# Performance work log

Measured on AMD Instinct MI355X. Metric: run time of the kernel, lower is better.

## Reference

```python
import jax, jax.numpy as jnp
import numpy as np

B, D_IN, T = 16, 512, 4096
D_CB, K = 8, 1024
COMMITMENT = 1.0


def _weight_norm(v, g):
    # torch weight_norm with dim=0: w[o] = g[o] * v[o] / ||v[o]||
    return g[:, None] * v / jnp.sqrt(jnp.sum(v * v, axis=1, keepdims=True))


def setup_inputs() -> dict:
    key = jax.random.key(0)
    ks = jax.random.split(key, 8)
    return {
        "z": jax.random.normal(ks[0], (B, D_IN, T), dtype=jnp.float32),
        "in_v": jax.random.normal(ks[1], (D_CB, D_IN), dtype=jnp.float32) * 0.05,
        "in_g": jax.random.uniform(ks[2], (D_CB,), dtype=jnp.float32, minval=0.5, maxval=1.5),
        "in_b": jax.random.normal(ks[3], (D_CB,), dtype=jnp.float32) * 0.01,
        "out_v": jax.random.normal(ks[4], (D_IN, D_CB), dtype=jnp.float32) * 0.05,
        "out_g": jax.random.uniform(ks[5], (D_IN,), dtype=jnp.float32, minval=0.5, maxval=1.5),
        "out_b": jax.random.normal(ks[6], (D_IN,), dtype=jnp.float32) * 0.01,
        "codebook": jax.random.normal(ks[7], (K, D_CB), dtype=jnp.float32),
    }


def reference(z, in_v, in_g, in_b, out_v, out_g, out_b, codebook):
    z = z.astype(jnp.float32)
    # in_project: weight-normed 1x1 conv == per-timestep linear [D_IN -> D_CB]
    w_in = _weight_norm(in_v, in_g)                       # [D_CB, D_IN]
    z_e = jnp.einsum('cd,bdt->bct', w_in, z) + in_b[None, :, None]  # [B, D_CB, T]

    enc = jnp.transpose(z_e, (0, 2, 1))                   # [B, T, D_CB]
    cb = codebook.astype(jnp.float32)                     # [K, D_CB]
    # squared euclidean distance via expansion
    d = (jnp.sum(enc * enc, axis=-1, keepdims=True)
         - 2.0 * jnp.einsum('btd,kd->btk', enc, cb)
         + jnp.sum(cb * cb, axis=-1)[None, None, :])      # [B, T, K]
    indices = jnp.argmin(d, axis=-1)                      # [B, T] int

    z_q = jnp.transpose(cb[indices], (0, 2, 1))           # [B, D_CB, T]
    commit_loss = jnp.mean((z_e - jax.lax.stop_gradient(z_q)) ** 2, axis=(1, 2)) * COMMITMENT  # [B]

    # straight-through estimator
    z_q_st = z_e + jax.lax.stop_gradient(z_q - z_e)

    w_out = _weight_norm(out_v, out_g)                    # [D_IN, D_CB]
    out = jnp.einsum('cd,bdt->bct', w_out, z_q_st) + out_b[None, :, None]  # [B, D_IN, T]
    return out, commit_loss, indices
```

## Files before the change

kernel.cpp:

```cpp
#include <hip/hip_runtime.h>
#include <math.h>

#define NB 16
#define DIN 512
#define TT 4096
#define DCB 8
#define KC 1024
#define NW 8
#define TC 128


__global__ __launch_bounds__(512) void vq_setup(
    const float* __restrict__ in_v, const float* __restrict__ in_g,
    const float* __restrict__ out_v, const float* __restrict__ out_g,
    const float* __restrict__ cb, float* __restrict__ ws)
{
    int tid = threadIdx.x;
    float* w_inT = ws;
    float* w_out = ws + 4096;
    float* cb2   = ws + 8192;

    {
        int c    = tid >> 6;
        int lane = tid & 63;
        const float* v = in_v + c * DIN;
        float s = 0.f;
        #pragma unroll
        for (int i = 0; i < DIN; i += 64) {
            float x = v[i + lane];
            s += x * x;
        }
        #pragma unroll
        for (int off = 32; off > 0; off >>= 1) s += __shfl_xor(s, off, 64);
        float sq = sqrtf(s);
        float g  = in_g[c];
        #pragma unroll
        for (int i = 0; i < DIN; i += 64) {
            int d = i + lane;
            w_inT[d * DCB + c] = (g * v[d]) / sq;
        }
    }
    {
        int o = tid;
        const float* v = out_v + o * DCB;
        float s = 0.f;
        #pragma unroll
        for (int c = 0; c < DCB; ++c) s += v[c] * v[c];
        float sq = sqrtf(s);
        float g  = out_g[o];
        #pragma unroll
        for (int c = 0; c < DCB; ++c) w_out[o * DCB + c] = (g * v[c]) / sq;
    }
    for (int k = tid; k < KC; k += 512) {
        const float* r = cb + k * DCB;
        float s = 0.f;
        #pragma unroll
        for (int c = 0; c < DCB; ++c) s += r[c] * r[c];
        cb2[k] = s;
    }
}

__global__ __launch_bounds__(512, 4) void vq_main(
    const float* __restrict__ z, const float* __restrict__ in_b,
    const float* __restrict__ out_b, const float* __restrict__ cb,
    const float* __restrict__ ws, float* __restrict__ ws_commit,
    float* __restrict__ out)
{
    __shared__ float s_cb[KC * DCB];
    __shared__ float s_cb2[KC];
    __shared__ float s_red[NW * DCB * TC];
    __shared__ float s_sd[NW][TC];
    __shared__ int   s_si[NW][TC];

    const float* w_inT = ws;
    const float* w_out = ws + 4096;

    int tid  = threadIdx.x;
    int w    = tid >> 6;
    int wu   = __builtin_amdgcn_readfirstlane(w);
    int lane = tid & 63;
    int blk  = blockIdx.x;
    int b    = blk >> 5;
    int t0   = (blk & 31) * TC;
    int tl   = 2 * lane;

    {
        float4 c0 = ((const float4*)cb)[tid];
        float4 c1 = ((const float4*)cb)[512 + tid];
        float4 c2 = ((const float4*)cb)[1024 + tid];
        float4 c3 = ((const float4*)cb)[1536 + tid];
        ((float4*)s_cb)[tid]        = c0;
        ((float4*)s_cb)[512 + tid]  = c1;
        ((float4*)s_cb)[1024 + tid] = c2;
        ((float4*)s_cb)[1536 + tid] = c3;
        if (tid < 256) {
            float4 q = ((const float4*)(ws + 8192))[tid];
            ((float4*)s_cb2)[tid] = q;
        }
    }

    const float* zp = z + (size_t)b * DIN * TT + t0 + tl;

    float ze0[DCB], ze1[DCB];
    #pragma unroll
    for (int c = 0; c < DCB; ++c) { ze0[c] = 0.f; ze1[c] = 0.f; }

    int d0 = wu * 64;
    for (int db = 0; db < 64; db += 8) {
        float2 v[8];
        #pragma unroll
        for (int j = 0; j < 8; ++j)
            v[j] = *(const float2*)(zp + (size_t)(d0 + db + j) * TT);
        #pragma unroll
        for (int j = 0; j < 8; ++j) {
            const float* wi = w_inT + (d0 + db + j) * DCB;
            #pragma unroll
            for (int c = 0; c < DCB; ++c) {
                ze0[c] = fmaf(wi[c], v[j].x, ze0[c]);
                ze1[c] = fmaf(wi[c], v[j].y, ze1[c]);
            }
        }
    }

    float* redw = s_red + w * DCB * TC;
    #pragma unroll
    for (int c = 0; c < DCB; ++c) {
        redw[c * TC + tl]     = ze0[c];
        redw[c * TC + tl + 1] = ze1[c];
    }
    __syncthreads();

    #pragma unroll
    for (int c = 0; c < DCB; ++c) {
        float s0 = 0.f, s1 = 0.f;
        #pragma unroll
        for (int w2 = 0; w2 < NW; ++w2) {
            s0 += s_red[(w2 * DCB + c) * TC + tl];
            s1 += s_red[(w2 * DCB + c) * TC + tl + 1];
        }
        ze0[c] = s0 + in_b[c];
        ze1[c] = s1 + in_b[c];
    }

    float enc20 = 0.f, enc21 = 0.f;
    #pragma unroll
    for (int c = 0; c < DCB; ++c) {
        enc20 += ze0[c] * ze0[c];
        enc21 += ze1[c] * ze1[c];
    }

    float best0 = 3.4e38f, best1 = 3.4e38f;
    int   bi0   = 0,       bi1   = 0;
    int   k0    = wu * 128;
    #pragma unroll 4
    for (int kk = 0; kk < 128; ++kk) {
        int k = k0 + kk;
        float4 r0 = ((const float4*)s_cb)[2 * k];
        float4 r1 = ((const float4*)s_cb)[2 * k + 1];
        float dot0 = fmaf(ze0[0], r0.x, fmaf(ze0[1], r0.y, fmaf(ze0[2], r0.z, fmaf(ze0[3], r0.w,
                     fmaf(ze0[4], r1.x, fmaf(ze0[5], r1.y, fmaf(ze0[6], r1.z, ze0[7] * r1.w)))))));
        float dot1 = fmaf(ze1[0], r0.x, fmaf(ze1[1], r0.y, fmaf(ze1[2], r0.z, fmaf(ze1[3], r0.w,
                     fmaf(ze1[4], r1.x, fmaf(ze1[5], r1.y, fmaf(ze1[6], r1.z, ze1[7] * r1.w)))))));
        float c2  = s_cb2[k];
        float dk0 = (enc20 - 2.0f * dot0) + c2;
        float dk1 = (enc21 - 2.0f * dot1) + c2;
        if (dk0 < best0) { best0 = dk0; bi0 = k; }
        if (dk1 < best1) { best1 = dk1; bi1 = k; }
    }
    s_sd[w][tl]     = best0;  s_si[w][tl]     = bi0;
    s_sd[w][tl + 1] = best1;  s_si[w][tl + 1] = bi1;
    __syncthreads();

    float g0 = s_sd[0][tl], g1 = s_sd[0][tl + 1];
    int  gi0 = s_si[0][tl], gi1 = s_si[0][tl + 1];
    #pragma unroll
    for (int w2 = 1; w2 < NW; ++w2) {
        float d0_ = s_sd[w2][tl],     d1_ = s_sd[w2][tl + 1];
        int   i0_ = s_si[w2][tl],     i1_ = s_si[w2][tl + 1];
        if (d0_ < g0) { g0 = d0_; gi0 = i0_; }
        if (d1_ < g1) { g1 = d1_; gi1 = i1_; }
    }

    float4 q0a = ((const float4*)s_cb)[2 * gi0], q0b = ((const float4*)s_cb)[2 * gi0 + 1];
    float4 q1a = ((const float4*)s_cb)[2 * gi1], q1b = ((const float4*)s_cb)[2 * gi1 + 1];

    if (wu == 0) {
        float cl = 0.f;
        float f;
        f = ze0[0]-q0a.x; cl = fmaf(f,f,cl);  f = ze1[0]-q1a.x; cl = fmaf(f,f,cl);
        f = ze0[1]-q0a.y; cl = fmaf(f,f,cl);  f = ze1[1]-q1a.y; cl = fmaf(f,f,cl);
        f = ze0[2]-q0a.z; cl = fmaf(f,f,cl);  f = ze1[2]-q1a.z; cl = fmaf(f,f,cl);
        f = ze0[3]-q0a.w; cl = fmaf(f,f,cl);  f = ze1[3]-q1a.w; cl = fmaf(f,f,cl);
        f = ze0[4]-q0b.x; cl = fmaf(f,f,cl);  f = ze1[4]-q1b.x; cl = fmaf(f,f,cl);
        f = ze0[5]-q0b.y; cl = fmaf(f,f,cl);  f = ze1[5]-q1b.y; cl = fmaf(f,f,cl);
        f = ze0[6]-q0b.z; cl = fmaf(f,f,cl);  f = ze1[6]-q1b.z; cl = fmaf(f,f,cl);
        f = ze0[7]-q0b.w; cl = fmaf(f,f,cl);  f = ze1[7]-q1b.w; cl = fmaf(f,f,cl);
        #pragma unroll
        for (int off = 32; off > 0; off >>= 1) cl += __shfl_xor(cl, off, 64);
        if (lane == 0) ws_commit[blk] = cl;
        float2 iv = make_float2((float)gi0, (float)gi1);
        *(float2*)(out + (size_t)NB * DIN * TT + NB + (size_t)b * TT + t0 + tl) = iv;
    }

    float* outp = out + (size_t)b * DIN * TT + t0 + tl;
    int o0 = wu * 64;
    #pragma unroll 4
    for (int oo = 0; oo < 64; ++oo) {
        int o = o0 + oo;
        const float* wo = w_out + o * DCB;
        float obias = out_b[o];
        float a0 = fmaf(wo[0], q0a.x, fmaf(wo[1], q0a.y, fmaf(wo[2], q0a.z, fmaf(wo[3], q0a.w,
                   fmaf(wo[4], q0b.x, fmaf(wo[5], q0b.y, fmaf(wo[6], q0b.z, wo[7] * q0b.w)))))));
        float a1 = fmaf(wo[0], q1a.x, fmaf(wo[1], q1a.y, fmaf(wo[2], q1a.z, fmaf(wo[3], q1a.w,
                   fmaf(wo[4], q1b.x, fmaf(wo[5], q1b.y, fmaf(wo[6], q1b.z, wo[7] * q1b.w)))))));
        *(float2*)(outp + (size_t)o * TT) = make_float2(a0 + obias, a1 + obias);
    }
}

__global__ __launch_bounds__(64) void vq_commit(
    const float* __restrict__ ws_commit, float* __restrict__ out)
{
    int b    = blockIdx.x;
    int lane = threadIdx.x;
    float s = (lane < 32) ? ws_commit[b * 32 + lane] : 0.f;
    #pragma unroll
    for (int off = 32; off > 0; off >>= 1) s += __shfl_xor(s, off, 64);
    if (lane == 0)
        out[(size_t)NB * DIN * TT + b] = s * (1.0f / (DCB * TT));
}

extern "C" void kernel_launch(void* const* d_in, const int* in_sizes, int n_in,
                              void* d_out, int out_size, void* d_ws, size_t ws_size,
                              hipStream_t stream) {
    const float* z     = (const float*)d_in[0];
    const float* in_v  = (const float*)d_in[1];
    const float* in_g  = (const float*)d_in[2];
    const float* in_b  = (const float*)d_in[3];
    const float* out_v = (const float*)d_in[4];
    const float* out_g = (const float*)d_in[5];
    const float* out_b = (const float*)d_in[6];
    const float* cb    = (const float*)d_in[7];

    float* ws  = (float*)d_ws;
    float* out = (float*)d_out;

    vq_setup<<<1, 512, 0, stream>>>(in_v, in_g, out_v, out_g, cb, ws);
    vq_main<<<512, 512, 0, stream>>>(z, in_b, out_b, cb, ws, ws + 9216, out);
    vq_commit<<<NB, 64, 0, stream>>>(ws + 9216, out);
}
```

Baseline: 70.53 us.

## Reuse LDS buffer for reduction and codebook, widen argmin register tile

The codebook shared-memory array and the cross-wave reduction buffer now share one region. The codebook is loaded into registers early and written to LDS only after the reduction, shrinking the block's LDS footprint. The reduction is restructured so each wave sums one channel, and z_e is stored in shared memory. The argmin loop now gives each lane 4 timesteps over 64 codes (16 slices) instead of 2 timesteps over 128 codes, reusing each codebook LDS read across more FMAs at the cost of more registers and an extra barrier.

```diff
diff --git a/kernel.cpp b/kernel.cpp
--- a/kernel.cpp
+++ b/kernel.cpp
@@ -66,11 +66,11 @@
     const float* __restrict__ ws, float* __restrict__ ws_commit,
     float* __restrict__ out)
 {
-    __shared__ float s_cb[KC * DCB];
+    __shared__ float s_buf[KC * DCB];
+    __shared__ float s_ze[DCB * TC];
     __shared__ float s_cb2[KC];
-    __shared__ float s_red[NW * DCB * TC];
-    __shared__ float s_sd[NW][TC];
-    __shared__ int   s_si[NW][TC];
+    __shared__ float s_sd[16][TC];
+    __shared__ int   s_si[16][TC];
 
     const float* w_inT = ws;
     const float* w_out = ws + 4096;
@@ -84,19 +84,9 @@
     int t0   = (blk & 31) * TC;
     int tl   = 2 * lane;
 
-    {
-        float4 c0 = ((const float4*)cb)[tid];
-        float4 c1 = ((const float4*)cb)[512 + tid];
-        float4 c2 = ((const float4*)cb)[1024 + tid];
-        float4 c3 = ((const float4*)cb)[1536 + tid];
-        ((float4*)s_cb)[tid]        = c0;
-        ((float4*)s_cb)[512 + tid]  = c1;
-        ((float4*)s_cb)[1024 + tid] = c2;
-        ((float4*)s_cb)[1536 + tid] = c3;
-        if (tid < 256) {
-            float4 q = ((const float4*)(ws + 8192))[tid];
-            ((float4*)s_cb2)[tid] = q;
-        }
+    if (tid < 256) {
+        float4 q = ((const float4*)(ws + 8192))[tid];
+        ((float4*)s_cb2)[tid] = q;
     }
 
     const float* zp = z + (size_t)b * DIN * TT + t0 + tl;
@@ -122,79 +112,109 @@
         }
     }
 
-    float* redw = s_red + w * DCB * TC;
-    #pragma unroll
-    for (int c = 0; c < DCB; ++c) {
-        redw[c * TC + tl]     = ze0[c];
-        redw[c * TC + tl + 1] = ze1[c];
-    }
-    __syncthreads();
-
-    #pragma unroll
-    for (int c = 0; c < DCB; ++c) {
-        float s0 = 0.f, s1 = 0.f;
+    {
+        float* redw = s_buf + w * (DCB * TC);
+        #pragma unroll
+        for (int c = 0; c < DCB; ++c)
+            *(float2*)(redw + c * TC + tl) = make_float2(ze0[c], ze1[c]);
+    }
+
+    float4 p0 = ((const float4*)cb)[tid];
+    float4 p1 = ((const float4*)cb)[512 + tid];
+    float4 p2 = ((const float4*)cb)[1024 + tid];
+    float4 p3 = ((const float4*)cb)[1536 + tid];
+
+    __syncthreads();
+
+    {
+        float sa = 0.f, sb = 0.f;
         #pragma unroll
         for (int w2 = 0; w2 < NW; ++w2) {
-            s0 += s_red[(w2 * DCB + c) * TC + tl];
-            s1 += s_red[(w2 * DCB + c) * TC + tl + 1];
-        }
-        ze0[c] = s0 + in_b[c];
-        ze1[c] = s1 + in_b[c];
-    }
-
-    float enc20 = 0.f, enc21 = 0.f;
-    #pragma unroll
-    for (int c = 0; c < DCB; ++c) {
-        enc20 += ze0[c] * ze0[c];
-        enc21 += ze1[c] * ze1[c];
-    }
-
-    float best0 = 3.4e38f, best1 = 3.4e38f;
-    int   bi0   = 0,       bi1   = 0;
-    int   k0    = wu * 128;
-    #pragma unroll 4
-    for (int kk = 0; kk < 128; ++kk) {
-        int k = k0 + kk;
-        float4 r0 = ((const float4*)s_cb)[2 * k];
-        float4 r1 = ((const float4*)s_cb)[2 * k + 1];
-        float dot0 = fmaf(ze0[0], r0.x, fmaf(ze0[1], r0.y, fmaf(ze0[2], r0.z, fmaf(ze0[3], r0.w,
-                     fmaf(ze0[4], r1.x, fmaf(ze0[5], r1.y, fmaf(ze0[6], r1.z, ze0[7] * r1.w)))))));
-        float dot1 = fmaf(ze1[0], r0.x, fmaf(ze1[1], r0.y, fmaf(ze1[2], r0.z, fmaf(ze1[3], r0.w,
-                     fmaf(ze1[4], r1.x, fmaf(ze1[5], r1.y, fmaf(ze1[6], r1.z, ze1[7] * r1.w)))))));
-        float c2  = s_cb2[k];
-        float dk0 = (enc20 - 2.0f * dot0) + c2;
-        float dk1 = (enc21 - 2.0f * dot1) + c2;
-        if (dk0 < best0) { best0 = dk0; bi0 = k; }
-        if (dk1 < best1) { best1 = dk1; bi1 = k; }
-    }
-    s_sd[w][tl]     = best0;  s_si[w][tl]     = bi0;
-    s_sd[w][tl + 1] = best1;  s_si[w][tl + 1] = bi1;
+            float2 r = *(const float2*)(s_buf + w2 * (DCB * TC) + w * TC + tl);
+            sa += r.x; sb += r.y;
+        }
+        float bias = in_b[w];
+        *(float2*)(s_ze + w * TC + tl) = make_float2(sa + bias, sb + bias);
+    }
+    __syncthreads();
+
+    ((float4*)s_buf)[tid]        = p0;
+    ((float4*)s_buf)[512 + tid]  = p1;
+    ((float4*)s_buf)[1024 + tid] = p2;
+    ((float4*)s_buf)[1536 + tid] = p3;
+    __syncthreads();
+
+    {
+        int h  = lane >> 5;
+        int t4 = 4 * (lane & 31);
+        int s  = 2 * w + h;
+        int k0 = 64 * s;
+
+        float zr[DCB][4];
+        #pragma unroll
+        for (int c = 0; c < DCB; ++c) {
+            float4 v = *(const float4*)(s_ze + c * TC + t4);
+            zr[c][0] = v.x; zr[c][1] = v.y; zr[c][2] = v.z; zr[c][3] = v.w;
+        }
+        float enc2[4];
+        #pragma unroll
+        for (int j = 0; j < 4; ++j) {
+            float e = 0.f;
+            #pragma unroll
+            for (int c = 0; c < DCB; ++c) e += zr[c][j] * zr[c][j];
+            enc2[j] = e;
+        }
+
+        float best[4] = {3.4e38f, 3.4e38f, 3.4e38f, 3.4e38f};
+        int   bi[4]   = {0, 0, 0, 0};
+        #pragma unroll 4
+        for (int kk = 0; kk < 64; ++kk) {
+            int k = k0 + kk;
+            float4 r0 = ((const float4*)s_buf)[2 * k];
+            float4 r1 = ((const float4*)s_buf)[2 * k + 1];
+            float c2  = s_cb2[k];
+            #pragma unroll
+            for (int j = 0; j < 4; ++j) {
+                float dot = fmaf(zr[0][j], r0.x, fmaf(zr[1][j], r0.y, fmaf(zr[2][j], r0.z, fmaf(zr[3][j], r0.w,
+                            fmaf(zr[4][j], r1.x, fmaf(zr[5][j], r1.y, fmaf(zr[6][j], r1.z, zr[7][j] * r1.w)))))));
+                float dk  = (enc2[j] - 2.0f * dot) + c2;
+                if (dk < best[j]) { best[j] = dk; bi[j] = k; }
+            }
+        }
+        *(float4*)(&s_sd[s][t4]) = make_float4(best[0], best[1], best[2], best[3]);
+        *(int4*)  (&s_si[s][t4]) = make_int4(bi[0], bi[1], bi[2], bi[3]);
+    }
     __syncthreads();
 
     float g0 = s_sd[0][tl], g1 = s_sd[0][tl + 1];
     int  gi0 = s_si[0][tl], gi1 = s_si[0][tl + 1];
     #pragma unroll
-    for (int w2 = 1; w2 < NW; ++w2) {
-        float d0_ = s_sd[w2][tl],     d1_ = s_sd[w2][tl + 1];
-        int   i0_ = s_si[w2][tl],     i1_ = s_si[w2][tl + 1];
+    for (int s2 = 1; s2 < 16; ++s2) {
+        float d0_ = s_sd[s2][tl],  d1_ = s_sd[s2][tl + 1];
+        int   i0_ = s_si[s2][tl],  i1_ = s_si[s2][tl + 1];
         if (d0_ < g0) { g0 = d0_; gi0 = i0_; }
         if (d1_ < g1) { g1 = d1_; gi1 = i1_; }
     }
 
-    float4 q0a = ((const float4*)s_cb)[2 * gi0], q0b = ((const float4*)s_cb)[2 * gi0 + 1];
-    float4 q1a = ((const float4*)s_cb)[2 * gi1], q1b = ((const float4*)s_cb)[2 * gi1 + 1];
+    float4 q0a = ((const float4*)s_buf)[2 * gi0], q0b = ((const float4*)s_buf)[2 * gi0 + 1];
+    float4 q1a = ((const float4*)s_buf)[2 * gi1], q1b = ((const float4*)s_buf)[2 * gi1 + 1];
 
     if (wu == 0) {
-        float cl = 0.f;
-        float f;
-        f = ze0[0]-q0a.x; cl = fmaf(f,f,cl);  f = ze1[0]-q1a.x; cl = fmaf(f,f,cl);
-        f = ze0[1]-q0a.y; cl = fmaf(f,f,cl);  f = ze1[1]-q1a.y; cl = fmaf(f,f,cl);
-        f = ze0[2]-q0a.z; cl = fmaf(f,f,cl);  f = ze1[2]-q1a.z; cl = fmaf(f,f,cl);
-        f = ze0[3]-q0a.w; cl = fmaf(f,f,cl);  f = ze1[3]-q1a.w; cl = fmaf(f,f,cl);
-        f = ze0[4]-q0b.x; cl = fmaf(f,f,cl);  f = ze1[4]-q1b.x; cl = fmaf(f,f,cl);
-        f = ze0[5]-q0b.y; cl = fmaf(f,f,cl);  f = ze1[5]-q1b.y; cl = fmaf(f,f,cl);
-        f = ze0[6]-q0b.z; cl = fmaf(f,f,cl);  f = ze1[6]-q1b.z; cl = fmaf(f,f,cl);
-        f = ze0[7]-q0b.w; cl = fmaf(f,f,cl);  f = ze1[7]-q1b.w; cl = fmaf(f,f,cl);
+        float zeA[DCB], zeB[DCB];
+        #pragma unroll
+        for (int c = 0; c < DCB; ++c) {
+            float2 zz = *(const float2*)(s_ze + c * TC + tl);
+            zeA[c] = zz.x; zeB[c] = zz.y;
+        }
+        float cl = 0.f, f;
+        f = zeA[0]-q0a.x; cl = fmaf(f,f,cl);  f = zeB[0]-q1a.x; cl = fmaf(f,f,cl);
+        f = zeA[1]-q0a.y; cl = fmaf(f,f,cl);  f = zeB[1]-q1a.y; cl = fmaf(f,f,cl);
+        f = zeA[2]-q0a.z; cl = fmaf(f,f,cl);  f = zeB[2]-q1a.z; cl = fmaf(f,f,cl);
+        f = zeA[3]-q0a.w; cl = fmaf(f,f,cl);  f = zeB[3]-q1a.w; cl = fmaf(f,f,cl);
+        f = zeA[4]-q0b.x; cl = fmaf(f,f,cl);  f = zeB[4]-q1b.x; cl = fmaf(f,f,cl);
+        f = zeA[5]-q0b.y; cl = fmaf(f,f,cl);  f = zeB[5]-q1b.y; cl = fmaf(f,f,cl);
+        f = zeA[6]-q0b.z; cl = fmaf(f,f,cl);  f = zeB[6]-q1b.z; cl = fmaf(f,f,cl);
+        f = zeA[7]-q0b.w; cl = fmaf(f,f,cl);  f = zeB[7]-q1b.w; cl = fmaf(f,f,cl);
         #pragma unroll
         for (int off = 32; off > 0; off >>= 1) cl += __shfl_xor(cl, off, 64);
         if (lane == 0) ws_commit[blk] = cl;
```

New measurement: 67.46 us. 1.05x faster.
